# Performance work log

Hardware: AMD Instinct MI355X
Metric: run time of the kernel (lower is better)

## Reference

```python
import jax, jax.numpy as jnp
import numpy as np

NEG_INF = jnp.float32(-9e15)

def gat_layer(x, adj_mask, W, a, alpha):
    # x: [N, F_in]; W: [H, F_in, F_out]; a: [H, 2*F_out]; adj_mask: [N, N] bool
    H, _, O = W.shape
    h = jnp.einsum('nf,hfo->hno', x, W)            # [H, N, O]
    a_src, a_dst = a[:, :O], a[:, O:]              # [H, O] each
    e_src = jnp.einsum('hno,ho->hn', h, a_src)     # [H, N]
    e_dst = jnp.einsum('hno,ho->hn', h, a_dst)     # [H, N]
    e = jax.nn.leaky_relu(e_src[:, :, None] + e_dst[:, None, :], negative_slope=alpha)
    e = jnp.where(adj_mask[None, :, :], e, NEG_INF)  # mask non-edges
    attn = jax.nn.softmax(e, axis=-1)              # [H, N, N]
    out = jnp.einsum('hnm,hmo->hno', attn, h)      # [H, N, O]
    return out.mean(axis=0)                        # average heads -> [N, O]

def setup_inputs() -> dict:
    key = jax.random.key(0)
    ks = jax.random.split(key, 6)
    N, F_IN, F_HID, F_CLS, H = 4096, 512, 256, 16, 4
    x = jax.random.normal(ks[0], (N, F_IN), dtype=jnp.float32)
    adj = jax.random.randint(ks[1], (N, N), 0, 2, dtype=jnp.int32)
    W1 = jax.random.normal(ks[2], (H, F_IN, F_HID), dtype=jnp.float32) * 0.05
    a1 = jax.random.normal(ks[3], (H, 2 * F_HID), dtype=jnp.float32) * 0.05
    W2 = jax.random.normal(ks[4], (1, F_HID, F_CLS), dtype=jnp.float32) * 0.05
    a2 = jax.random.normal(ks[5], (1, 2 * F_CLS), dtype=jnp.float32) * 0.05
    return {"x": x, "adj": adj, "W1": W1, "a1": a1, "W2": W2, "a2": a2}

def reference(x, adj, W1, a1, W2, a2):
    alpha = 0.2
    adj_mask = adj > 0
    h = jax.nn.relu(gat_layer(x, adj_mask, W1, a1, alpha))        # layer1 + ReLU
    out = gat_layer(h, adj_mask, W2, a2, alpha)                    # layer2
    return jax.nn.log_softmax(out, axis=1)                         # [N, nclass]
```

## Files before the change

kernel.cpp:

```cpp
#include <hip/hip_runtime.h>
#include <stdint.h>

#define N_NODES 4096
#define F_IN    512
#define F_HID   256
#define F_CLS   16
#define NHEAD   4
#define ALPHA   0.2f
#define LOG2E   1.4426950408889634f

typedef __attribute__((ext_vector_type(8))) short short8;
typedef __attribute__((ext_vector_type(4))) float f32x4;

__device__ __forceinline__ float bf2f(unsigned short h) {
    unsigned u = ((unsigned)h) << 16; float f; __builtin_memcpy(&f, &u, 4); return f;
}
__device__ __forceinline__ unsigned short f2bf(float f) {
    unsigned u; __builtin_memcpy(&u, &f, 4);
    u += 0x7fffu + ((u >> 16) & 1u);
    return (unsigned short)(u >> 16);
}
__device__ __forceinline__ float lo_bf(unsigned u) { u <<= 16;          float f; __builtin_memcpy(&f,&u,4); return f; }
__device__ __forceinline__ float hi_bf(unsigned u) { u &= 0xffff0000u;  float f; __builtin_memcpy(&f,&u,4); return f; }

__device__ __forceinline__ void async_cp16(void* lds, const void* g) {
    __builtin_amdgcn_global_load_lds(
        (const __attribute__((address_space(1))) unsigned int*)g,
        (__attribute__((address_space(3))) unsigned int*)lds,
        16, 0, 0);
}

__device__ __forceinline__ void pipe_barrier_vm3() {
    __builtin_amdgcn_sched_barrier(0);
    __builtin_amdgcn_s_waitcnt(0x0073);
    __builtin_amdgcn_s_barrier();
    __builtin_amdgcn_sched_barrier(0);
}
__device__ __forceinline__ void pipe_barrier_vm4() {
    __builtin_amdgcn_sched_barrier(0);
    __builtin_amdgcn_s_waitcnt(0x0074);
    __builtin_amdgcn_s_barrier();
    __builtin_amdgcn_sched_barrier(0);
}

#define PREP_BM_BLOCKS   16384
#define PREP_CV_BLOCKS   1296
#define PREP_Z_BLOCKS    4
__global__ __launch_bounds__(256) void k_prep(const int* __restrict__ adj,
                                              const float* __restrict__ x,
                                              const float* __restrict__ W1,
                                              const float* __restrict__ W2,
                                              unsigned long long* __restrict__ bm,
                                              unsigned short* __restrict__ xb,
                                              unsigned short* __restrict__ W1t,
                                              float* __restrict__ W2t,
                                              float* __restrict__ ez) {
    int b = blockIdx.x;
    if (b < PREP_BM_BLOCKS) {
        int wv = threadIdx.x >> 6, lane = threadIdx.x & 63;
        int idx0 = b * 1024 + wv * 256;
        const int* p = adj + idx0 + lane;
        unsigned long long m0 = __ballot(p[0]   > 0);
        unsigned long long m1 = __ballot(p[64]  > 0);
        unsigned long long m2 = __ballot(p[128] > 0);
        unsigned long long m3 = __ballot(p[192] > 0);
        if (lane == 0) {
            int w = idx0 >> 6;
            bm[w] = m0; bm[w+1] = m1; bm[w+2] = m2; bm[w+3] = m3;
        }
        return;
    }
    if (b < PREP_BM_BLOCKS + PREP_CV_BLOCKS) {
        int tid = (b - PREP_BM_BLOCKS) * 256 + threadIdx.x;
        const int NXV = (N_NODES * F_IN) / 8;
        const int NW1 = NHEAD * 64 * F_HID;
        if (tid < NXV) {
            float4 a = *(const float4*)&x[tid * 8];
            float4 c = *(const float4*)&x[tid * 8 + 4];
            uint4 w;
            w.x = (unsigned)f2bf(a.x) | ((unsigned)f2bf(a.y) << 16);
            w.y = (unsigned)f2bf(a.z) | ((unsigned)f2bf(a.w) << 16);
            w.z = (unsigned)f2bf(c.x) | ((unsigned)f2bf(c.y) << 16);
            w.w = (unsigned)f2bf(c.z) | ((unsigned)f2bf(c.w) << 16);
            *(uint4*)&xb[tid * 8] = w;
        } else if (tid < NXV + NW1) {
            int j = tid - NXV;
            int o = j & 255, f8 = (j >> 8) & 63, h = j >> 14;
            float v[8];
            #pragma unroll
            for (int k = 0; k < 8; ++k)
                v[k] = W1[(size_t)(h * F_IN + f8 * 8 + k) * F_HID + o];
            uint4 w;
            w.x = (unsigned)f2bf(v[0]) | ((unsigned)f2bf(v[1]) << 16);
            w.y = (unsigned)f2bf(v[2]) | ((unsigned)f2bf(v[3]) << 16);
            w.z = (unsigned)f2bf(v[4]) | ((unsigned)f2bf(v[5]) << 16);
            w.w = (unsigned)f2bf(v[6]) | ((unsigned)f2bf(v[7]) << 16);
            *(uint4*)&W1t[(size_t)(h * F_HID + o) * F_IN + f8 * 8] = w;
        } else {
            int j = tid - NXV - NW1;
            if (j < F_HID * F_CLS) {
                int o = j >> 4, c = j & 15;
                W2t[c * F_HID + o] = W2[j];
            }
        }
        return;
    }
    {
        int zb = b - PREP_BM_BLOCKS - PREP_CV_BLOCKS;
        float4* z4 = (float4*)ez;
        #pragma unroll
        for (int r = 0; r < 8; ++r)
            z4[zb * 2048 + r * 256 + threadIdx.x] = make_float4(0.f, 0.f, 0.f, 0.f);
    }
}

__global__ __launch_bounds__(256, 4) void k_gemm1(const unsigned short* __restrict__ xb,
                                                  const unsigned short* __restrict__ W1t,
                                                  const float* __restrict__ a1,
                                                  unsigned short* __restrict__ h1t,
                                                  float* __restrict__ es1,
                                                  float* __restrict__ ed1) {
    __shared__ unsigned short Sld[3][6144];
    const int t = threadIdx.x;
    const int lane = t & 63, wv = t >> 6, quad = lane >> 4, l15 = lane & 15;
    const int wn = wv & 1, wo = wv >> 1;
    const int n0 = blockIdx.x * 128;
    const int oo0 = blockIdx.y * 64;
    const int h = blockIdx.z;
    const int kl = (lane >> 4) * 8;

    const unsigned short* gs[3];
    int loff[3];
    #pragma unroll
    for (int s = 0; s < 3; ++s) {
        int c = wv * 3 + s;
        loff[s] = c * 512;
        gs[s] = (c < 8)
            ? (xb  + (size_t)(n0 + c * 16 + l15) * F_IN + kl)
            : (W1t + (size_t)(h * F_HID + oo0 + (c - 8) * 16 + l15) * F_IN + kl);
    }
    #pragma unroll
    for (int s = 0; s < 3; ++s) async_cp16(&Sld[0][loff[s]], gs[s]);
    #pragma unroll
    for (int s = 0; s < 3; ++s) async_cp16(&Sld[1][loff[s]], gs[s] + 32);

    f32x4 acc[4][2] = {};
    int cur = 0;
    for (int it = 0; it < 16; ++it) {
        pipe_barrier_vm3();
        {
            const int nxt = (cur >= 1) ? cur - 1 : 2;
            const int off = ((it + 2) & 15) * 32;
            #pragma unroll
            for (int s = 0; s < 3; ++s) async_cp16(&Sld[nxt][loff[s]], gs[s] + off);
        }
        short8 bfw[2];
        #pragma unroll
        for (int mi = 0; mi < 2; ++mi)
            bfw[mi] = *(const short8*)&Sld[cur][(8 + wo * 2 + mi) * 512 + lane * 8];
        #pragma unroll
        for (int ni = 0; ni < 4; ++ni) {
            short8 af = *(const short8*)&Sld[cur][(wn * 4 + ni) * 512 + lane * 8];
            #pragma unroll
            for (int mi = 0; mi < 2; ++mi)
                acc[ni][mi] = __builtin_amdgcn_mfma_f32_16x16x32_bf16(af, bfw[mi], acc[ni][mi], 0, 0, 0);
        }
        cur = (cur == 2) ? 0 : cur + 1;
    }
    #pragma unroll
    for (int ni = 0; ni < 4; ++ni)
      #pragma unroll
      for (int mi = 0; mi < 2; ++mi) {
        int o = oo0 + wo * 32 + mi * 16 + l15;
        int nb = n0 + wn * 64 + ni * 16 + quad * 4;
        uint2 uu;
        uu.x = (unsigned)f2bf(acc[ni][mi][0]) | ((unsigned)f2bf(acc[ni][mi][1]) << 16);
        uu.y = (unsigned)f2bf(acc[ni][mi][2]) | ((unsigned)f2bf(acc[ni][mi][3]) << 16);
        *(uint2*)&h1t[(size_t)(h * F_HID + o) * N_NODES + nb] = uu;
      }
    float a1s[2], a1d[2];
    #pragma unroll
    for (int mi = 0; mi < 2; ++mi) {
        int o = oo0 + wo * 32 + mi * 16 + l15;
        a1s[mi] = a1[h * 2 * F_HID + o] * LOG2E;
        a1d[mi] = a1[h * 2 * F_HID + F_HID + o] * LOG2E;
    }
    #pragma unroll
    for (int ni = 0; ni < 4; ++ni) {
        #pragma unroll
        for (int rg = 0; rg < 4; ++rg) {
            float es = acc[ni][0][rg] * a1s[0] + acc[ni][1][rg] * a1s[1];
            float ed = acc[ni][0][rg] * a1d[0] + acc[ni][1][rg] * a1d[1];
            #pragma unroll
            for (int off = 1; off < 16; off <<= 1) {
                es += __shfl_xor(es, off, 64);
                ed += __shfl_xor(ed, off, 64);
            }
            if (l15 == 0) {
                int n = n0 + wn * 64 + ni * 16 + quad * 4 + rg;
                atomicAdd(&es1[h * N_NODES + n], es);
                atomicAdd(&ed1[h * N_NODES + n], ed);
            }
        }
    }
}

__global__ __launch_bounds__(512, 2) void k_attn1(const unsigned short* __restrict__ h1t,
                                                  const float* __restrict__ es1,
                                                  const float* __restrict__ ed1,
                                                  const unsigned char* __restrict__ bmb,
                                                  unsigned short* __restrict__ C1p,
                                                  float* __restrict__ l1p) {
    __shared__ unsigned short Bld[3][16384];
    const int t = threadIdx.x;
    const int lane = t & 63, wv = t >> 6, quad = lane >> 4, l15 = lane & 15;
    const int m0 = blockIdx.x * 256;
    const int h = blockIdx.y;
    const int kz = blockIdx.z;
    const int mb0 = kz * 1024;

    const int m_r0 = m0 + wv * 32 + l15;
    const int m_r1 = m_r0 + 16;
    const float esr0 = es1[h * N_NODES + m_r0];
    const float esr1 = es1[h * N_NODES + m_r1];
    const unsigned char* bp0 = bmb + (size_t)m_r0 * (N_NODES / 8) + (mb0 >> 3);
    const unsigned char* bp1 = bmb + (size_t)m_r1 * (N_NODES / 8) + (mb0 >> 3);
    const float* edb = ed1 + h * N_NODES + mb0;

    const unsigned short* gb0 = h1t + (size_t)(h * F_HID + wv * 16 + l15) * N_NODES + mb0 + quad * 8;
    const unsigned short* gb1 = h1t + (size_t)(h * F_HID + (wv + 8) * 16 + l15) * N_NODES + mb0 + quad * 8;
    #pragma unroll
    for (int st = 0; st < 2; ++st) {
        async_cp16(&Bld[st][wv * 512],              gb0 + st * 64);
        async_cp16(&Bld[st][(wv + 8) * 512],        gb1 + st * 64);
        async_cp16(&Bld[st][8192 + wv * 512],       gb0 + st * 64 + 32);
        async_cp16(&Bld[st][8192 + (wv + 8) * 512], gb1 + st * 64 + 32);
    }

    f32x4 acc[16][2] = {};
    float lsum0 = 0.f, lsum1 = 0.f;
    int cur = 0;
    for (int p = 0; p < 16; ++p) {
        pipe_barrier_vm4();
        {
            const int nxt = (cur >= 1) ? cur - 1 : 2;
            const int joff = ((p + 2) & 15) * 64;
            async_cp16(&Bld[nxt][wv * 512],              gb0 + joff);
            async_cp16(&Bld[nxt][(wv + 8) * 512],        gb1 + joff);
            async_cp16(&Bld[nxt][8192 + wv * 512],       gb0 + joff + 32);
            async_cp16(&Bld[nxt][8192 + (wv + 8) * 512], gb1 + joff + 32);
        }
        #pragma unroll
        for (int jh = 0; jh < 2; ++jh) {
            const int mb = p * 64 + jh * 32;
            float4 e0 = *(const float4*)&edb[mb + quad * 8];
            float4 e1v = *(const float4*)&edb[mb + quad * 8 + 4];
            float ev[8] = {e0.x, e0.y, e0.z, e0.w, e1v.x, e1v.y, e1v.z, e1v.w};
            unsigned bb0 = bp0[(mb >> 3) + quad];
            unsigned bb1 = bp1[(mb >> 3) + quad];
            unsigned up0[8], up1[8];
            #pragma unroll
            for (int j = 0; j < 8; ++j) {
                float s0 = esr0 + ev[j]; s0 = fmaxf(s0, ALPHA * s0);
                float p0 = ((bb0 >> j) & 1u) ? __builtin_amdgcn_exp2f(s0) : 0.f;
                unsigned u0; __builtin_memcpy(&u0, &p0, 4); u0 &= 0xffff0000u;
                float pt0; __builtin_memcpy(&pt0, &u0, 4);
                lsum0 += pt0; up0[j] = u0;
                float s1 = esr1 + ev[j]; s1 = fmaxf(s1, ALPHA * s1);
                float p1 = ((bb1 >> j) & 1u) ? __builtin_amdgcn_exp2f(s1) : 0.f;
                unsigned u1; __builtin_memcpy(&u1, &p1, 4); u1 &= 0xffff0000u;
                float pt1; __builtin_memcpy(&pt1, &u1, 4);
                lsum1 += pt1; up1[j] = u1;
            }
            int pk0[4], pk1[4];
            #pragma unroll
            for (int j = 0; j < 4; ++j) {
                pk0[j] = __builtin_amdgcn_perm(up0[2*j+1], up0[2*j], 0x07060302u);
                pk1[j] = __builtin_amdgcn_perm(up1[2*j+1], up1[2*j], 0x07060302u);
            }
            short8 bfrag0, bfrag1;
            __builtin_memcpy(&bfrag0, pk0, 16);
            __builtin_memcpy(&bfrag1, pk1, 16);
            #pragma unroll
            for (int ot = 0; ot < 16; ++ot) {
                short8 af = *(const short8*)&Bld[cur][jh * 8192 + ot * 512 + lane * 8];
                acc[ot][0] = __builtin_amdgcn_mfma_f32_16x16x32_bf16(af, bfrag0, acc[ot][0], 0, 0, 0);
                acc[ot][1] = __builtin_amdgcn_mfma_f32_16x16x32_bf16(af, bfrag1, acc[ot][1], 0, 0, 0);
            }
        }
        cur = (cur == 2) ? 0 : cur + 1;
    }
    lsum0 += __shfl_xor(lsum0, 16, 64); lsum0 += __shfl_xor(lsum0, 32, 64);
    lsum1 += __shfl_xor(lsum1, 16, 64); lsum1 += __shfl_xor(lsum1, 32, 64);
    if (quad == 0) {
        l1p[(size_t)(kz * NHEAD + h) * N_NODES + m_r0] = lsum0;
        l1p[(size_t)(kz * NHEAD + h) * N_NODES + m_r1] = lsum1;
    }
    unsigned short* Cb = C1p + (size_t)(kz * NHEAD + h) * N_NODES * F_HID;
    #pragma unroll
    for (int ot = 0; ot < 16; ++ot)
      #pragma unroll
      for (int mi = 0; mi < 2; ++mi) {
        int m = (mi == 0) ? m_r0 : m_r1;
        int o0 = ot * 16 + quad * 4;
        uint2 uu;
        uu.x = (unsigned)f2bf(acc[ot][mi][0]) | ((unsigned)f2bf(acc[ot][mi][1]) << 16);
        uu.y = (unsigned)f2bf(acc[ot][mi][2]) | ((unsigned)f2bf(acc[ot][mi][3]) << 16);
        *(uint2*)&Cb[(size_t)m * F_HID + o0] = uu;
      }
}

__global__ __launch_bounds__(256) void k_reduce_h2w(const unsigned short* __restrict__ C1p,
                                                    const float* __restrict__ l1p,
                                                    const float* __restrict__ W2t,
                                                    const float* __restrict__ a2,
                                                    unsigned short* __restrict__ h2wt,
                                                    float* __restrict__ es2,
                                                    float* __restrict__ ed2) {
    __shared__ float h2s[8][256];
    int t = threadIdx.x;
    int og = t & 31, nl = t >> 5;
    int n = blockIdx.x * 8 + nl;
    float acc8[8] = {};
    #pragma unroll
    for (int h = 0; h < NHEAD; ++h) {
        float den = 0.f, num[8] = {};
        #pragma unroll
        for (int kz = 0; kz < 4; ++kz) {
            den += l1p[(size_t)(kz * NHEAD + h) * N_NODES + n];
            uint4 u = *(const uint4*)&C1p[((size_t)(kz * NHEAD + h) * N_NODES + n) * F_HID + og * 8];
            num[0] += lo_bf(u.x); num[1] += hi_bf(u.x);
            num[2] += lo_bf(u.y); num[3] += hi_bf(u.y);
            num[4] += lo_bf(u.z); num[5] += hi_bf(u.z);
            num[6] += lo_bf(u.w); num[7] += hi_bf(u.w);
        }
        float rinv = 1.f / fmaxf(den, 1e-30f);
        #pragma unroll
        for (int j = 0; j < 8; ++j) acc8[j] += num[j] * rinv;
    }
    #pragma unroll
    for (int j = 0; j < 8; ++j) {
        float v = fmaxf(acc8[j] * 0.25f, 0.f);
        h2s[nl][og * 8 + j] = bf2f(f2bf(v));
    }
    __syncthreads();
    if (t < 128) {
        int c = t & 15, n2l = t >> 4;
        int n2 = blockIdx.x * 8 + n2l;
        const float* wrow = W2t + c * F_HID;
        const float* hrow = h2s[n2l];
        float dot = 0.f;
        #pragma unroll 4
        for (int o = 0; o < F_HID; o += 8) {
            float4 hv0 = *(const float4*)&hrow[o];
            float4 hv1 = *(const float4*)&hrow[o + 4];
            float4 w0 = *(const float4*)&wrow[o];
            float4 w1 = *(const float4*)&wrow[o + 4];
            dot += hv0.x*w0.x + hv0.y*w0.y + hv0.z*w0.z + hv0.w*w0.w;
            dot += hv1.x*w1.x + hv1.y*w1.y + hv1.z*w1.z + hv1.w*w1.w;
        }
        h2wt[(size_t)c * N_NODES + n2] = f2bf(dot);
        float es = dot * a2[c] * LOG2E;
        float ed = dot * a2[F_CLS + c] * LOG2E;
        #pragma unroll
        for (int off = 1; off < 16; off <<= 1) {
            es += __shfl_xor(es, off, 64);
            ed += __shfl_xor(ed, off, 64);
        }
        if (c == 0) { es2[n2] = es; ed2[n2] = ed; }
    }
}

__global__ __launch_bounds__(256, 4) void k_attn2(const unsigned short* __restrict__ h2wt,
                                                  const float* __restrict__ es2,
                                                  const float* __restrict__ ed2,
                                                  const unsigned char* __restrict__ bmb,
                                                  float* __restrict__ out2p,
                                                  float* __restrict__ l2p) {
    const int t = threadIdx.x;
    const int lane = t & 63, wv = t >> 6, quad = lane >> 4, l15 = lane & 15;
    const int m0 = blockIdx.x * 64;
    const int ks = blockIdx.y;
    const int m_r = m0 + wv * 16 + l15;
    const float esr = es2[m_r];
    const unsigned char* bp = bmb + (size_t)m_r * (N_NODES / 8);

    f32x4 acc = {};
    float lsum = 0.f;
    for (int it = 0; it < 16; ++it) {
        const int mb = ks * 512 + it * 32;
        float4 e0 = *(const float4*)&ed2[mb + quad * 8];
        float4 e1v = *(const float4*)&ed2[mb + quad * 8 + 4];
        float ev[8] = {e0.x, e0.y, e0.z, e0.w, e1v.x, e1v.y, e1v.z, e1v.w};
        unsigned bb = bp[(mb >> 3) + quad];
        short8 afrag;
        #pragma unroll
        for (int j = 0; j < 8; ++j) {
            float s = esr + ev[j]; s = fmaxf(s, ALPHA * s);
            float p = ((bb >> j) & 1u) ? __builtin_amdgcn_exp2f(s) : 0.f;
            lsum += p; afrag[j] = (short)f2bf(p);
        }
        short8 bfr = *(const short8*)&h2wt[(size_t)l15 * N_NODES + mb + quad * 8];
        acc = __builtin_amdgcn_mfma_f32_16x16x32_bf16(afrag, bfr, acc, 0, 0, 0);
    }
    lsum += __shfl_xor(lsum, 16, 64); lsum += __shfl_xor(lsum, 32, 64);
    if (quad == 0) l2p[(size_t)ks * N_NODES + m_r] = lsum;
    #pragma unroll
    for (int rg = 0; rg < 4; ++rg) {
        int row = m0 + wv * 16 + quad * 4 + rg;
        out2p[((size_t)ks * N_NODES + row) * F_CLS + l15] = acc[rg];
    }
}

__global__ __launch_bounds__(256) void k_final(const float* __restrict__ out2p,
                                               const float* __restrict__ l2p,
                                               float* __restrict__ out) {
    int t = threadIdx.x;
    int c = t & 15, nl = t >> 4;
    int n = blockIdx.x * 16 + nl;
    float v = 0.f, l = 0.f;
    #pragma unroll
    for (int ks = 0; ks < 8; ++ks) {
        v += out2p[((size_t)ks * N_NODES + n) * F_CLS + c];
        l += l2p[(size_t)ks * N_NODES + n];
    }
    v /= fmaxf(l, 1e-30f);
    float mx = v;
    #pragma unroll
    for (int off = 1; off < 16; off <<= 1) mx = fmaxf(mx, __shfl_xor(mx, off, 64));
    float e = __expf(v - mx);
    float se = e;
    #pragma unroll
    for (int off = 1; off < 16; off <<= 1) se += __shfl_xor(se, off, 64);
    out[(size_t)n * F_CLS + c] = v - mx - __logf(se);
}

#define OFF_BM    0ull
#define OFF_XB    2097152ull
#define OFF_W1T   6291456ull
#define OFF_W2T   7340032ull
#define OFF_ES1   7356416ull
#define OFF_ED1   7421952ull
#define OFF_ES2   7487488ull
#define OFF_ED2   7503872ull
#define OFF_L1P   7520256ull
#define OFF_L2P   7782400ull
#define OFF_OUT2P 7910400ull
#define OFF_H2WT  10007552ull
#define OFF_H1T   10138624ull
#define OFF_C1P   18527232ull

extern "C" void kernel_launch(void* const* d_in, const int* in_sizes, int n_in,
                              void* d_out, int out_size, void* d_ws, size_t ws_size,
                              hipStream_t stream) {
    const float* x   = (const float*)d_in[0];
    const int*   adj = (const int*)d_in[1];
    const float* W1  = (const float*)d_in[2];
    const float* a1  = (const float*)d_in[3];
    const float* W2  = (const float*)d_in[4];
    const float* a2  = (const float*)d_in[5];
    float* out = (float*)d_out;
    char* ws = (char*)d_ws;

    unsigned long long* bm  = (unsigned long long*)(ws + OFF_BM);
    unsigned char*      bmb = (unsigned char*)(ws + OFF_BM);
    unsigned short* xb   = (unsigned short*)(ws + OFF_XB);
    unsigned short* W1t  = (unsigned short*)(ws + OFF_W1T);
    float* W2t   = (float*)(ws + OFF_W2T);
    float* es1   = (float*)(ws + OFF_ES1);
    float* ed1   = (float*)(ws + OFF_ED1);
    float* es2   = (float*)(ws + OFF_ES2);
    float* ed2   = (float*)(ws + OFF_ED2);
    float* l1p   = (float*)(ws + OFF_L1P);
    float* l2p   = (float*)(ws + OFF_L2P);
    float* out2p = (float*)(ws + OFF_OUT2P);
    unsigned short* h2wt = (unsigned short*)(ws + OFF_H2WT);
    unsigned short* h1t  = (unsigned short*)(ws + OFF_H1T);
    unsigned short* C1p  = (unsigned short*)(ws + OFF_C1P);

    k_prep       <<<dim3(PREP_BM_BLOCKS + PREP_CV_BLOCKS + PREP_Z_BLOCKS), 256, 0, stream>>>(
                     adj, x, W1, W2, bm, xb, W1t, W2t, es1);
    k_gemm1      <<<dim3(32, 4, 4), 256, 0, stream>>>(xb, W1t, a1, h1t, es1, ed1);
    k_attn1      <<<dim3(16, 4, 4), 512, 0, stream>>>(h1t, es1, ed1, bmb, C1p, l1p);
    k_reduce_h2w <<<dim3(512),      256, 0, stream>>>(C1p, l1p, W2t, a2, h2wt, es2, ed2);
    k_attn2      <<<dim3(64, 8),    256, 0, stream>>>(h2wt, es2, ed2, bmb, out2p, l2p);
    k_final      <<<dim3(256),      256, 0, stream>>>(out2p, l2p, out);
}
```

Baseline: 222.7 us.

## Fold adjacency bitmask build into gemm1 grid and prefetch attn2 operands

Building the adjacency bitmask is moved out of the prep kernel and into extra blocks appended to the gemm1 grid. The bandwidth-bound read of the large int adjacency matrix can then run alongside the compute-bound projection GEMM instead of before it. k_attn2 is also software-pipelined: it loads the next iteration's ed2, h2wt and bitmask words one step ahead and reads the bitmask 16 bytes at a time. The prefetch reads a little past each row's slice of the bitmask, and the extra blocks compete with gemm1 for CU slots.

```diff
diff --git a/kernel.cpp b/kernel.cpp
--- a/kernel.cpp
+++ b/kernel.cpp
@@ -43,35 +43,18 @@
     __builtin_amdgcn_sched_barrier(0);
 }
 
-#define PREP_BM_BLOCKS   16384
 #define PREP_CV_BLOCKS   1296
 #define PREP_Z_BLOCKS    4
-__global__ __launch_bounds__(256) void k_prep(const int* __restrict__ adj,
-                                              const float* __restrict__ x,
+__global__ __launch_bounds__(256) void k_prep(const float* __restrict__ x,
                                               const float* __restrict__ W1,
                                               const float* __restrict__ W2,
-                                              unsigned long long* __restrict__ bm,
                                               unsigned short* __restrict__ xb,
                                               unsigned short* __restrict__ W1t,
                                               float* __restrict__ W2t,
                                               float* __restrict__ ez) {
     int b = blockIdx.x;
-    if (b < PREP_BM_BLOCKS) {
-        int wv = threadIdx.x >> 6, lane = threadIdx.x & 63;
-        int idx0 = b * 1024 + wv * 256;
-        const int* p = adj + idx0 + lane;
-        unsigned long long m0 = __ballot(p[0]   > 0);
-        unsigned long long m1 = __ballot(p[64]  > 0);
-        unsigned long long m2 = __ballot(p[128] > 0);
-        unsigned long long m3 = __ballot(p[192] > 0);
-        if (lane == 0) {
-            int w = idx0 >> 6;
-            bm[w] = m0; bm[w+1] = m1; bm[w+2] = m2; bm[w+3] = m3;
-        }
-        return;
-    }
-    if (b < PREP_BM_BLOCKS + PREP_CV_BLOCKS) {
-        int tid = (b - PREP_BM_BLOCKS) * 256 + threadIdx.x;
+    if (b < PREP_CV_BLOCKS) {
+        int tid = b * 256 + threadIdx.x;
         const int NXV = (N_NODES * F_IN) / 8;
         const int NW1 = NHEAD * 64 * F_HID;
         if (tid < NXV) {
@@ -106,7 +89,7 @@
         return;
     }
     {
-        int zb = b - PREP_BM_BLOCKS - PREP_CV_BLOCKS;
+        int zb = b - PREP_CV_BLOCKS;
         float4* z4 = (float4*)ez;
         #pragma unroll
         for (int r = 0; r < 8; ++r)
@@ -119,8 +102,25 @@
                                                   const float* __restrict__ a1,
                                                   unsigned short* __restrict__ h1t,
                                                   float* __restrict__ es1,
-                                                  float* __restrict__ ed1) {
+                                                  float* __restrict__ ed1,
+                                                  const int* __restrict__ adj,
+                                                  unsigned long long* __restrict__ bm) {
     __shared__ unsigned short Sld[3][6144];
+    if (blockIdx.x >= 32) {
+        int unit = (blockIdx.x - 32) * 16 + blockIdx.y * 4 + blockIdx.z;
+        int wv = threadIdx.x >> 6, lane = threadIdx.x & 63;
+        int idx0 = unit * 1024 + wv * 256;
+        const int* p = adj + idx0 + lane;
+        unsigned long long m0 = __ballot(p[0]   > 0);
+        unsigned long long m1 = __ballot(p[64]  > 0);
+        unsigned long long m2 = __ballot(p[128] > 0);
+        unsigned long long m3 = __ballot(p[192] > 0);
+        if (lane == 0) {
+            int w = idx0 >> 6;
+            bm[w] = m0; bm[w+1] = m1; bm[w+2] = m2; bm[w+3] = m3;
+        }
+        return;
+    }
     const int t = threadIdx.x;
     const int lane = t & 63, wv = t >> 6, quad = lane >> 4, l15 = lane & 15;
     const int wn = wv & 1, wo = wv >> 1;
@@ -381,27 +381,44 @@
     const int lane = t & 63, wv = t >> 6, quad = lane >> 4, l15 = lane & 15;
     const int m0 = blockIdx.x * 64;
     const int ks = blockIdx.y;
+    const int mb0 = ks * 512;
     const int m_r = m0 + wv * 16 + l15;
     const float esr = es2[m_r];
-    const unsigned char* bp = bmb + (size_t)m_r * (N_NODES / 8);
+    const unsigned char* bp = bmb + (size_t)m_r * (N_NODES / 8) + (mb0 >> 3);
+    const float* edb = ed2 + mb0;
+    const unsigned short* hb = h2wt + (size_t)l15 * N_NODES + mb0 + quad * 8;
+
+    uint4 bq = *(const uint4*)bp;
+    float4 e0 = *(const float4*)&edb[quad * 8];
+    float4 e1 = *(const float4*)&edb[quad * 8 + 4];
+    short8 bfr = *(const short8*)&hb[0];
 
     f32x4 acc = {};
     float lsum = 0.f;
-    for (int it = 0; it < 16; ++it) {
-        const int mb = ks * 512 + it * 32;
-        float4 e0 = *(const float4*)&ed2[mb + quad * 8];
-        float4 e1v = *(const float4*)&ed2[mb + quad * 8 + 4];
-        float ev[8] = {e0.x, e0.y, e0.z, e0.w, e1v.x, e1v.y, e1v.z, e1v.w};
-        unsigned bb = bp[(mb >> 3) + quad];
-        short8 afrag;
-        #pragma unroll
-        for (int j = 0; j < 8; ++j) {
-            float s = esr + ev[j]; s = fmaxf(s, ALPHA * s);
-            float p = ((bb >> j) & 1u) ? __builtin_amdgcn_exp2f(s) : 0.f;
-            lsum += p; afrag[j] = (short)f2bf(p);
-        }
-        short8 bfr = *(const short8*)&h2wt[(size_t)l15 * N_NODES + mb + quad * 8];
-        acc = __builtin_amdgcn_mfma_f32_16x16x32_bf16(afrag, bfr, acc, 0, 0, 0);
+    for (int it4 = 0; it4 < 4; ++it4) {
+        uint4 nbq;
+        #pragma unroll
+        for (int sub = 0; sub < 4; ++sub) {
+            const int it = it4 * 4 + sub;
+            const int itn = (it + 1) & 15;
+            float4 ne0 = *(const float4*)&edb[itn * 32 + quad * 8];
+            float4 ne1 = *(const float4*)&edb[itn * 32 + quad * 8 + 4];
+            short8 nbf = *(const short8*)&hb[itn * 32];
+            if (sub == 0) nbq = *(const uint4*)(bp + (it4 + 1) * 16);
+            const unsigned d[4] = {bq.x, bq.y, bq.z, bq.w};
+            unsigned bb = (d[sub] >> (quad * 8)) & 0xffu;
+            float ev[8] = {e0.x, e0.y, e0.z, e0.w, e1.x, e1.y, e1.z, e1.w};
+            short8 afrag;
+            #pragma unroll
+            for (int j = 0; j < 8; ++j) {
+                float s = esr + ev[j]; s = fmaxf(s, ALPHA * s);
+                float p = ((bb >> j) & 1u) ? __builtin_amdgcn_exp2f(s) : 0.f;
+                lsum += p; afrag[j] = (short)f2bf(p);
+            }
+            acc = __builtin_amdgcn_mfma_f32_16x16x32_bf16(afrag, bfr, acc, 0, 0, 0);
+            e0 = ne0; e1 = ne1; bfr = nbf;
+            if (sub == 3) bq = nbq;
+        }
     }
     lsum += __shfl_xor(lsum, 16, 64); lsum += __shfl_xor(lsum, 32, 64);
     if (quad == 0) l2p[(size_t)ks * N_NODES + m_r] = lsum;
@@ -478,9 +495,9 @@
     unsigned short* h1t  = (unsigned short*)(ws + OFF_H1T);
     unsigned short* C1p  = (unsigned short*)(ws + OFF_C1P);
 
-    k_prep       <<<dim3(PREP_BM_BLOCKS + PREP_CV_BLOCKS + PREP_Z_BLOCKS), 256, 0, stream>>>(
-                     adj, x, W1, W2, bm, xb, W1t, W2t, es1);
-    k_gemm1      <<<dim3(32, 4, 4), 256, 0, stream>>>(xb, W1t, a1, h1t, es1, ed1);
+    k_prep       <<<dim3(PREP_CV_BLOCKS + PREP_Z_BLOCKS), 256, 0, stream>>>(
+                     x, W1, W2, xb, W1t, W2t, es1);
+    k_gemm1      <<<dim3(32 + 1024, 4, 4), 256, 0, stream>>>(xb, W1t, a1, h1t, es1, ed1, adj, bm);
     k_attn1      <<<dim3(16, 4, 4), 512, 0, stream>>>(h1t, es1, ed1, bmb, C1p, l1p);
     k_reduce_h2w <<<dim3(512),      256, 0, stream>>>(C1p, l1p, W2t, a2, h2wt, es2, ed2);
     k_attn2      <<<dim3(64, 8),    256, 0, stream>>>(h2wt, es2, ed2, bmb, out2p, l2p);
```

Result: slower. 234.8 us (+5.4%).
